# Optimization experiments

Measured on AMD Instinct MI355X. Metric: run time of the kernel, lower is better.

The kernel has to match this reference:

```python
import jax, jax.numpy as jnp
import numpy as np

NEG_SLOPE = 0.2  # PyG GATConv default LeakyReLU slope
EPS = 1e-16


def gat_layer(x, W, a_src, a_dst, bias, src, dst, heads, out_dim, concat):
    N = x.shape[0]
    h = (x @ W).reshape(N, heads, out_dim)          # [N,H,C]
    alpha_src = (h * a_src).sum(-1)                  # [N,H]
    alpha_dst = (h * a_dst).sum(-1)                  # [N,H]
    e = jax.nn.leaky_relu(alpha_src[src] + alpha_dst[dst], NEG_SLOPE)  # [E,H]
    # segment softmax over incoming edges of each destination node
    m = jax.ops.segment_max(e, dst, num_segments=N)  # [N,H]
    p = jnp.exp(e - m[dst])
    denom = jax.ops.segment_sum(p, dst, num_segments=N)
    alpha = p / (denom[dst] + EPS)                   # [E,H]
    # scatter-aggregate messages to destinations
    out = jax.ops.segment_sum(alpha[:, :, None] * h[src], dst, num_segments=N)  # [N,H,C]
    out = out.reshape(N, heads * out_dim) if concat else out.mean(axis=1)
    return out + bias


def setup_inputs() -> dict:
    N, E, F_IN, NC = 100000, 1600000, 512, 10
    key = jax.random.key(0)
    ks = jax.random.split(key, 9)
    return {
        "x": jax.random.normal(ks[0], (N, F_IN), jnp.float32),
        "W1": jax.random.normal(ks[1], (F_IN, 64), jnp.float32) * (1.0 / np.sqrt(F_IN)),
        "att_src1": jax.random.normal(ks[2], (1, 8, 8), jnp.float32) * 0.1,
        "att_dst1": jax.random.normal(ks[3], (1, 8, 8), jnp.float32) * 0.1,
        "b1": jnp.zeros((64,), jnp.float32),
        "W2": jax.random.normal(ks[4], (64, NC), jnp.float32) * (1.0 / 8.0),
        "att_src2": jax.random.normal(ks[5], (1, 1, NC), jnp.float32) * 0.1,
        "att_dst2": jax.random.normal(ks[6], (1, 1, NC), jnp.float32) * 0.1,
        "b2": jnp.zeros((NC,), jnp.float32),
        "edge_index": jax.random.randint(ks[7], (2, E), 0, N, jnp.int64),
    }


def reference(x, W1, att_src1, att_dst1, b1, W2, att_src2, att_dst2, b2, edge_index):
    N = x.shape[0]
    # add self-loops (PyG GATConv add_self_loops=True default)
    loop = jnp.arange(N, dtype=edge_index.dtype)
    src = jnp.concatenate([edge_index[0], loop])
    dst = jnp.concatenate([edge_index[1], loop])
    h = gat_layer(x, W1, att_src1, att_dst1, b1, src, dst, heads=8, out_dim=8, concat=True)
    h = jax.nn.elu(h)
    nc = W2.shape[1]
    out = gat_layer(h, W2, att_src2, att_dst2, b2, src, dst, heads=1, out_dim=nc, concat=False)
    return jax.nn.log_softmax(out, axis=1)
```

## Files before the change

### kernel.cpp

```cpp
#include <hip/hip_runtime.h>
#include <math.h>

#define NEG 0.2f

typedef __bf16 bf16x8 __attribute__((ext_vector_type(8)));
typedef __bf16 bf16x4 __attribute__((ext_vector_type(4)));
typedef float  f32x4  __attribute__((ext_vector_type(4)));

__global__ void histw1_k(const int* __restrict__ ei, int E, int Nn,
                         int* __restrict__ deg, int* __restrict__ rank,
                         const float* __restrict__ W1, __bf16* __restrict__ W1b)
{
    if (blockIdx.x < 16) {
        int i = blockIdx.x * 256 + threadIdx.x;
        int n = i & 63;
        int k0 = (i >> 6) * 8;
#pragma unroll
        for (int j = 0; j < 8; ++j)
            W1b[(size_t)i * 8 + j] = (__bf16)W1[(size_t)(k0 + j) * 64 + n];
        return;
    }
    int e = (blockIdx.x - 16) * 256 + threadIdx.x;
    int Ep = E + Nn;
    if (e >= Ep) return;
    int d = (e < E) ? ei[E + e] : e - E;
    rank[e] = atomicAdd(&deg[d], 1);
}

__global__ void scan_a_k(const int* __restrict__ deg, int Nn, int* __restrict__ bsum)
{
    __shared__ int tmp[256];
    int t = threadIdx.x;
    int base = blockIdx.x * 1024 + t * 4;
    int s = 0;
#pragma unroll
    for (int j = 0; j < 4; ++j) { int i = base + j; if (i < Nn) s += deg[i]; }
    tmp[t] = s;
    __syncthreads();
    for (int off = 1; off < 256; off <<= 1) {
        int a = (t >= off) ? tmp[t - off] : 0;
        __syncthreads();
        tmp[t] += a;
        __syncthreads();
    }
    if (t == 255) bsum[blockIdx.x] = tmp[255];
}

__global__ void scan_b_k(int* __restrict__ bsum, int nb)
{
    __shared__ int tmp[256];
    int t = threadIdx.x;
    int v = (t < nb) ? bsum[t] : 0;
    tmp[t] = v;
    __syncthreads();
    for (int off = 1; off < 256; off <<= 1) {
        int a = (t >= off) ? tmp[t - off] : 0;
        __syncthreads();
        tmp[t] += a;
        __syncthreads();
    }
    if (t < nb) bsum[t] = tmp[t] - v;
}

__global__ void scan_c_k(const int* __restrict__ deg, int Nn, const int* __restrict__ boff,
                         int* __restrict__ rowptr)
{
    __shared__ int tmp[256];
    int t = threadIdx.x;
    int base = blockIdx.x * 1024 + t * 4;
    int v[4];
    int s = 0;
#pragma unroll
    for (int j = 0; j < 4; ++j) {
        int i = base + j;
        v[j] = (i < Nn) ? deg[i] : 0;
        s += v[j];
    }
    tmp[t] = s;
    __syncthreads();
    for (int off = 1; off < 256; off <<= 1) {
        int a = (t >= off) ? tmp[t - off] : 0;
        __syncthreads();
        tmp[t] += a;
        __syncthreads();
    }
    int excl = boff[blockIdx.x] + tmp[t] - s;
#pragma unroll
    for (int j = 0; j < 4; ++j) {
        int i = base + j;
        if (i < Nn) {
            rowptr[i] = excl;
            excl += v[j];
            if (i == Nn - 1) rowptr[Nn] = excl;
        }
    }
}

__global__ __launch_bounds__(256, 4) void scatgemm_k(
    const float* __restrict__ x, const __bf16* __restrict__ W1b,
    const float* __restrict__ asrc, const float* __restrict__ adst,
    __bf16* __restrict__ h1b, float* __restrict__ as1, float* __restrict__ ad1,
    const int* __restrict__ ei, int E,
    const int* __restrict__ rowptr, const int* __restrict__ rank,
    int* __restrict__ csr, int Nn, int nbG)
{
    if ((int)blockIdx.x >= nbG) {
        int e = ((int)blockIdx.x - nbG) * 256 + threadIdx.x;
        int Ep = E + Nn;
        if (e >= Ep) return;
        int s, d;
        if (e < E) { s = ei[e]; d = ei[E + e]; } else { s = d = e - E; }
        csr[rowptr[d] + rank[e]] = s;
        return;
    }
    int t = threadIdx.x;
    int wave = t >> 6, lane = t & 63;
    int lm = lane & 15, lk = lane >> 4;
    int rowa = blockIdx.x * 64 + wave * 16 + lm;
    const float* xrow = x + (size_t)(rowa < Nn ? rowa : 0) * 512;
    f32x4 acc[4] = {};
#pragma unroll
    for (int ch = 0; ch < 16; ++ch) {
        float4 a0 = *(const float4*)(xrow + ch * 32 + lk * 8);
        float4 a1 = *(const float4*)(xrow + ch * 32 + lk * 8 + 4);
        bf16x8 af;
        af[0] = (__bf16)a0.x; af[1] = (__bf16)a0.y;
        af[2] = (__bf16)a0.z; af[3] = (__bf16)a0.w;
        af[4] = (__bf16)a1.x; af[5] = (__bf16)a1.y;
        af[6] = (__bf16)a1.z; af[7] = (__bf16)a1.w;
#pragma unroll
        for (int nt = 0; nt < 4; ++nt) {
            bf16x8 bf = *(const bf16x8*)(W1b + ((size_t)((ch * 4 + lk) * 64) + nt * 16 + lm) * 8);
            acc[nt] = __builtin_amdgcn_mfma_f32_16x16x32_bf16(af, bf, acc[nt], 0, 0, 0);
        }
    }
    int rowbase = blockIdx.x * 64 + wave * 16 + lk * 4;
#pragma unroll
    for (int nt = 0; nt < 4; ++nt) {
#pragma unroll
        for (int j = 0; j < 4; ++j) {
            int gr = rowbase + j;
            if (gr < Nn) h1b[(size_t)gr * 64 + nt * 16 + lm] = (__bf16)acc[nt][j];
        }
    }
#pragma unroll
    for (int nt = 0; nt < 4; ++nt) {
        float ws = asrc[nt * 16 + lm];
        float wd = adst[nt * 16 + lm];
#pragma unroll
        for (int j = 0; j < 4; ++j) {
            float sv = acc[nt][j] * ws;
            float dv = acc[nt][j] * wd;
            sv += __shfl_xor(sv, 1); dv += __shfl_xor(dv, 1);
            sv += __shfl_xor(sv, 2); dv += __shfl_xor(dv, 2);
            sv += __shfl_xor(sv, 4); dv += __shfl_xor(dv, 4);
            int gr = rowbase + j;
            if ((lm & 7) == 0 && gr < Nn) {
                int hh = nt * 2 + (lm >> 3);
                as1[(size_t)gr * 8 + hh] = sv;
                ad1[(size_t)gr * 8 + hh] = dv;
            }
        }
    }
}

__global__ __launch_bounds__(256, 4) void agg1n_k(const int* __restrict__ csr,
                                                  const int* __restrict__ rowptr,
                                                  const float* __restrict__ as1,
                                                  const float* __restrict__ ad1,
                                                  const __bf16* __restrict__ h1b,
                                                  const float* __restrict__ b1,
                                                  const float* __restrict__ W2,
                                                  const float* __restrict__ as2w,
                                                  const float* __restrict__ ad2w,
                                                  float* __restrict__ h2,
                                                  float* __restrict__ as2,
                                                  float* __restrict__ ad2, int Nn)
{
    __shared__ float W2s[640];
    for (int i = threadIdx.x; i < 640; i += 256) W2s[i] = W2[i];
    __syncthreads();

    int wid = (blockIdx.x * 256 + threadIdx.x) >> 6;
    if (wid >= Nn) return;
    int lane = threadIdx.x & 63;
    int sub = lane >> 4;
    int c4 = lane & 15;
    int h = c4 >> 1;
    float adv = ad1[wid * 8 + h];
    int start = rowptr[wid];
    int len = rowptr[wid + 1] - start;
    float accp = 0.f;
    float4 accv = make_float4(0.f, 0.f, 0.f, 0.f);
    int i = sub;
    for (; i + 12 < len; i += 16) {
        int s0 = csr[start + i];
        int s1 = csr[start + i + 4];
        int s2 = csr[start + i + 8];
        int s3 = csr[start + i + 12];
        float e0 = as1[s0 * 8 + h] + adv;
        float e1 = as1[s1 * 8 + h] + adv;
        float e2 = as1[s2 * 8 + h] + adv;
        float e3 = as1[s3 * 8 + h] + adv;
        bf16x4 hv0 = *(const bf16x4*)(h1b + (size_t)s0 * 64 + c4 * 4);
        bf16x4 hv1 = *(const bf16x4*)(h1b + (size_t)s1 * 64 + c4 * 4);
        bf16x4 hv2 = *(const bf16x4*)(h1b + (size_t)s2 * 64 + c4 * 4);
        bf16x4 hv3 = *(const bf16x4*)(h1b + (size_t)s3 * 64 + c4 * 4);
        e0 = e0 > 0.f ? e0 : NEG * e0;
        e1 = e1 > 0.f ? e1 : NEG * e1;
        e2 = e2 > 0.f ? e2 : NEG * e2;
        e3 = e3 > 0.f ? e3 : NEG * e3;
        float p0 = __expf(e0), p1 = __expf(e1), p2 = __expf(e2), p3 = __expf(e3);
        accp += (p0 + p1) + (p2 + p3);
        accv.x += p0 * (float)hv0[0] + p1 * (float)hv1[0] + p2 * (float)hv2[0] + p3 * (float)hv3[0];
        accv.y += p0 * (float)hv0[1] + p1 * (float)hv1[1] + p2 * (float)hv2[1] + p3 * (float)hv3[1];
        accv.z += p0 * (float)hv0[2] + p1 * (float)hv1[2] + p2 * (float)hv2[2] + p3 * (float)hv3[2];
        accv.w += p0 * (float)hv0[3] + p1 * (float)hv1[3] + p2 * (float)hv2[3] + p3 * (float)hv3[3];
    }
    for (; i < len; i += 4) {
        int s0 = csr[start + i];
        float e0 = as1[s0 * 8 + h] + adv;
        bf16x4 hv0 = *(const bf16x4*)(h1b + (size_t)s0 * 64 + c4 * 4);
        e0 = e0 > 0.f ? e0 : NEG * e0;
        float p0 = __expf(e0);
        accp += p0;
        accv.x += p0 * (float)hv0[0];
        accv.y += p0 * (float)hv0[1];
        accv.z += p0 * (float)hv0[2];
        accv.w += p0 * (float)hv0[3];
    }
    accp   += __shfl_xor(accp, 16);
    accv.x += __shfl_xor(accv.x, 16);
    accv.y += __shfl_xor(accv.y, 16);
    accv.z += __shfl_xor(accv.z, 16);
    accv.w += __shfl_xor(accv.w, 16);
    accp   += __shfl_xor(accp, 32);
    accv.x += __shfl_xor(accv.x, 32);
    accv.y += __shfl_xor(accv.y, 32);
    accv.z += __shfl_xor(accv.z, 32);
    accv.w += __shfl_xor(accv.w, 32);

    float inv = 1.f / (accp + 1e-16f);
    float4 b = *(const float4*)(b1 + c4 * 4);
    float g0 = accv.x * inv + b.x; g0 = g0 > 0.f ? g0 : expm1f(g0);
    float g1 = accv.y * inv + b.y; g1 = g1 > 0.f ? g1 : expm1f(g1);
    float g2 = accv.z * inv + b.z; g2 = g2 > 0.f ? g2 : expm1f(g2);
    float g3 = accv.w * inv + b.w; g3 = g3 > 0.f ? g3 : expm1f(g3);
    int k0 = c4 * 4;
    float aj[10];
#pragma unroll
    for (int j = 0; j < 10; ++j)
        aj[j] = g0 * W2s[(k0 + 0) * 10 + j] + g1 * W2s[(k0 + 1) * 10 + j]
              + g2 * W2s[(k0 + 2) * 10 + j] + g3 * W2s[(k0 + 3) * 10 + j];
#pragma unroll
    for (int m = 1; m <= 8; m <<= 1) {
#pragma unroll
        for (int j = 0; j < 10; ++j) aj[j] += __shfl_xor(aj[j], m);
    }
    if (lane == 0) {
        float s2 = 0.f, d2 = 0.f;
#pragma unroll
        for (int j = 0; j < 10; ++j) { s2 += aj[j] * as2w[j]; d2 += aj[j] * ad2w[j]; }
        *(float4*)(h2 + (size_t)wid * 16 + 0) = make_float4(aj[0], aj[1], aj[2], aj[3]);
        *(float4*)(h2 + (size_t)wid * 16 + 4) = make_float4(aj[4], aj[5], aj[6], aj[7]);
        h2[(size_t)wid * 16 + 8] = aj[8];
        h2[(size_t)wid * 16 + 9] = aj[9];
        as2[wid] = s2;
        ad2[wid] = d2;
    }
}

__global__ __launch_bounds__(256) void agg2l_k(const int* __restrict__ csr,
                                               const int* __restrict__ rowptr,
                                               const float* __restrict__ as2,
                                               const float* __restrict__ ad2,
                                               const float* __restrict__ h2,
                                               const float* __restrict__ b2,
                                               float* __restrict__ out, int Nn)
{
    int wid = (blockIdx.x * 256 + threadIdx.x) >> 6;
    if (wid >= Nn) return;
    int lane = threadIdx.x & 63;
    int sub = lane >> 4;
    int c = lane & 15;
    float adv = ad2[wid];
    int start = rowptr[wid];
    int len = rowptr[wid + 1] - start;
    float accp = 0.f, accv = 0.f;
    int i = sub;
    for (; i + 12 < len; i += 16) {
        int s0 = csr[start + i];
        int s1 = csr[start + i + 4];
        int s2 = csr[start + i + 8];
        int s3 = csr[start + i + 12];
        float e0 = as2[s0] + adv;
        float e1 = as2[s1] + adv;
        float e2 = as2[s2] + adv;
        float e3 = as2[s3] + adv;
        float v0 = (c < 10) ? h2[(size_t)s0 * 16 + c] : 0.f;
        float v1 = (c < 10) ? h2[(size_t)s1 * 16 + c] : 0.f;
        float v2 = (c < 10) ? h2[(size_t)s2 * 16 + c] : 0.f;
        float v3 = (c < 10) ? h2[(size_t)s3 * 16 + c] : 0.f;
        e0 = e0 > 0.f ? e0 : NEG * e0;
        e1 = e1 > 0.f ? e1 : NEG * e1;
        e2 = e2 > 0.f ? e2 : NEG * e2;
        e3 = e3 > 0.f ? e3 : NEG * e3;
        float p0 = __expf(e0), p1 = __expf(e1), p2 = __expf(e2), p3 = __expf(e3);
        accp += (p0 + p1) + (p2 + p3);
        accv += p0 * v0 + p1 * v1 + p2 * v2 + p3 * v3;
    }
    for (; i < len; i += 4) {
        int s0 = csr[start + i];
        float e0 = as2[s0] + adv;
        float v0 = (c < 10) ? h2[(size_t)s0 * 16 + c] : 0.f;
        e0 = e0 > 0.f ? e0 : NEG * e0;
        float p0 = __expf(e0);
        accp += p0;
        accv += p0 * v0;
    }
    accp += __shfl_xor(accp, 16);
    accv += __shfl_xor(accv, 16);
    accp += __shfl_xor(accp, 32);
    accv += __shfl_xor(accv, 32);

    float z = (c < 10) ? accv / (accp + 1e-16f) + b2[c] : -1e30f;
    float m = z;
    m = fmaxf(m, __shfl_xor(m, 1));
    m = fmaxf(m, __shfl_xor(m, 2));
    m = fmaxf(m, __shfl_xor(m, 4));
    m = fmaxf(m, __shfl_xor(m, 8));
    float p = (c < 10) ? expf(z - m) : 0.f;
    p += __shfl_xor(p, 1);
    p += __shfl_xor(p, 2);
    p += __shfl_xor(p, 4);
    p += __shfl_xor(p, 8);
    float lse = m + logf(p);
    if (sub == 0 && c < 10)
        out[(size_t)wid * 10 + c] = z - lse;
}

extern "C" void kernel_launch(void* const* d_in, const int* in_sizes, int n_in,
                              void* d_out, int out_size, void* d_ws, size_t ws_size,
                              hipStream_t stream)
{
    const float* x     = (const float*)d_in[0];
    const float* W1    = (const float*)d_in[1];
    const float* asrc1 = (const float*)d_in[2];
    const float* adst1 = (const float*)d_in[3];
    const float* b1    = (const float*)d_in[4];
    const float* W2    = (const float*)d_in[5];
    const float* asrc2 = (const float*)d_in[6];
    const float* adst2 = (const float*)d_in[7];
    const float* b2    = (const float*)d_in[8];
    const int*   ei    = (const int*)d_in[9];
    float* out = (float*)d_out;

    int F  = in_sizes[1] / 64;
    int Nn = in_sizes[0] / F;
    int E  = in_sizes[9] / 2;
    int Ep = E + Nn;
    int nb = (Nn + 1023) / 1024;

    float* f = (float*)d_ws;
    __bf16* w1b = (__bf16*)f;  f += 512 * 64 / 2;
    __bf16* h1b = (__bf16*)f;  f += (size_t)Nn * 32;
    float* as1  = f;  f += (size_t)Nn * 8;
    float* ad1  = f;  f += (size_t)Nn * 8;
    float* h2   = f;  f += (size_t)Nn * 16;
    float* as2  = f;  f += Nn;
    float* ad2  = f;  f += Nn;
    int* ip = (int*)f;
    int* deg    = ip;  ip += Nn;
    int* rowptr = ip;  ip += Nn + 1;
    int* bsum   = ip;  ip += 256;
    int* rank   = ip;  ip += Ep;
    int* csr    = ip;  ip += Ep;

    int nbG = (Nn + 63) / 64;
    int nbS = (Ep + 255) / 256;

    hipMemsetAsync(deg, 0, (size_t)Nn * sizeof(int), stream);
    histw1_k<<<16 + nbS, 256, 0, stream>>>(ei, E, Nn, deg, rank, W1, w1b);

    scan_a_k<<<nb, 256, 0, stream>>>(deg, Nn, bsum);
    scan_b_k<<<1, 256, 0, stream>>>(bsum, nb);
    scan_c_k<<<nb, 256, 0, stream>>>(deg, Nn, bsum, rowptr);

    scatgemm_k<<<nbG + nbS, 256, 0, stream>>>(x, w1b, asrc1, adst1, h1b, as1, ad1,
                                              ei, E, rowptr, rank, csr, Nn, nbG);

    agg1n_k<<<(Nn + 3) / 4, 256, 0, stream>>>(csr, rowptr, as1, ad1, h1b,
                                              b1, W2, asrc2, adst2, h2, as2, ad2, Nn);

    agg2l_k<<<(Nn + 3) / 4, 256, 0, stream>>>(csr, rowptr, as2, ad2, h2, b2, out, Nn);
}
```

Baseline: 570.4 us.

## Widen per-lane gather vectors in aggregation kernels and split fused scatter/GEMM launch

Both aggregation kernels now give each lane a wider slice of the feature row, 8 bf16 values in layer 1 and 2 floats in layer 2. Eight edges are processed in parallel per wave, with a single masked 4-way unrolled loop replacing the unrolled loop plus tail loop. This is meant to cut the number of gather instructions and improve memory-level parallelism on the random neighbor reads, at the cost of more registers and wasted work on masked tail edges. The previously fused CSR-scatter/GEMM launch is split into two separate kernels, which removes the branch divergence between block types but adds a launch and loses the overlap between them.

```diff
diff --git a/kernel.cpp b/kernel.cpp
--- a/kernel.cpp
+++ b/kernel.cpp
@@ -4,7 +4,6 @@
 #define NEG 0.2f
 
 typedef __bf16 bf16x8 __attribute__((ext_vector_type(8)));
-typedef __bf16 bf16x4 __attribute__((ext_vector_type(4)));
 typedef float  f32x4  __attribute__((ext_vector_type(4)));
 
 __global__ void histw1_k(const int* __restrict__ ei, int E, int Nn,
@@ -96,23 +95,26 @@
     }
 }
 
-__global__ __launch_bounds__(256, 4) void scatgemm_k(
-    const float* __restrict__ x, const __bf16* __restrict__ W1b,
-    const float* __restrict__ asrc, const float* __restrict__ adst,
-    __bf16* __restrict__ h1b, float* __restrict__ as1, float* __restrict__ ad1,
-    const int* __restrict__ ei, int E,
-    const int* __restrict__ rowptr, const int* __restrict__ rank,
-    int* __restrict__ csr, int Nn, int nbG)
-{
-    if ((int)blockIdx.x >= nbG) {
-        int e = ((int)blockIdx.x - nbG) * 256 + threadIdx.x;
-        int Ep = E + Nn;
-        if (e >= Ep) return;
-        int s, d;
-        if (e < E) { s = ei[e]; d = ei[E + e]; } else { s = d = e - E; }
-        csr[rowptr[d] + rank[e]] = s;
-        return;
-    }
+__global__ void scat2_k(const int* __restrict__ ei, int E, int Nn,
+                        const int* __restrict__ rowptr, const int* __restrict__ rank,
+                        int* __restrict__ csr)
+{
+    int e = blockIdx.x * 256 + threadIdx.x;
+    int Ep = E + Nn;
+    if (e >= Ep) return;
+    int s, d;
+    if (e < E) { s = ei[e]; d = ei[E + e]; } else { s = d = e - E; }
+    csr[rowptr[d] + rank[e]] = s;
+}
+
+__global__ __launch_bounds__(256, 4) void gemm1a_k(const float* __restrict__ x,
+                                                   const __bf16* __restrict__ W1b,
+                                                   const float* __restrict__ asrc,
+                                                   const float* __restrict__ adst,
+                                                   __bf16* __restrict__ h1b,
+                                                   float* __restrict__ as1,
+                                                   float* __restrict__ ad1, int Nn)
+{
     int t = threadIdx.x;
     int wave = t >> 6, lane = t & 63;
     int lm = lane & 15, lk = lane >> 4;
@@ -184,76 +186,74 @@
     int wid = (blockIdx.x * 256 + threadIdx.x) >> 6;
     if (wid >= Nn) return;
     int lane = threadIdx.x & 63;
-    int sub = lane >> 4;
-    int c4 = lane & 15;
-    int h = c4 >> 1;
-    float adv = ad1[wid * 8 + h];
+    int sub = lane >> 3;
+    int c8  = lane & 7;
+    float advh = ad1[(size_t)wid * 8 + c8];
     int start = rowptr[wid];
     int len = rowptr[wid + 1] - start;
     float accp = 0.f;
-    float4 accv = make_float4(0.f, 0.f, 0.f, 0.f);
-    int i = sub;
-    for (; i + 12 < len; i += 16) {
-        int s0 = csr[start + i];
-        int s1 = csr[start + i + 4];
-        int s2 = csr[start + i + 8];
-        int s3 = csr[start + i + 12];
-        float e0 = as1[s0 * 8 + h] + adv;
-        float e1 = as1[s1 * 8 + h] + adv;
-        float e2 = as1[s2 * 8 + h] + adv;
-        float e3 = as1[s3 * 8 + h] + adv;
-        bf16x4 hv0 = *(const bf16x4*)(h1b + (size_t)s0 * 64 + c4 * 4);
-        bf16x4 hv1 = *(const bf16x4*)(h1b + (size_t)s1 * 64 + c4 * 4);
-        bf16x4 hv2 = *(const bf16x4*)(h1b + (size_t)s2 * 64 + c4 * 4);
-        bf16x4 hv3 = *(const bf16x4*)(h1b + (size_t)s3 * 64 + c4 * 4);
+    float accv[8] = {};
+    for (int i = sub; i < len; i += 32) {
+        int idx = start + i;
+        bool k1 = i + 8 < len, k2 = i + 16 < len, k3 = i + 24 < len;
+        int s0 = csr[idx];
+        int s1 = csr[idx + (k1 ? 8 : 0)];
+        int s2 = csr[idx + (k2 ? 16 : 0)];
+        int s3 = csr[idx + (k3 ? 24 : 0)];
+        float e0 = as1[(size_t)s0 * 8 + c8] + advh;
+        float e1 = as1[(size_t)s1 * 8 + c8] + advh;
+        float e2 = as1[(size_t)s2 * 8 + c8] + advh;
+        float e3 = as1[(size_t)s3 * 8 + c8] + advh;
+        bf16x8 hv0 = *(const bf16x8*)(h1b + (size_t)s0 * 64 + c8 * 8);
+        bf16x8 hv1 = *(const bf16x8*)(h1b + (size_t)s1 * 64 + c8 * 8);
+        bf16x8 hv2 = *(const bf16x8*)(h1b + (size_t)s2 * 64 + c8 * 8);
+        bf16x8 hv3 = *(const bf16x8*)(h1b + (size_t)s3 * 64 + c8 * 8);
         e0 = e0 > 0.f ? e0 : NEG * e0;
         e1 = e1 > 0.f ? e1 : NEG * e1;
         e2 = e2 > 0.f ? e2 : NEG * e2;
         e3 = e3 > 0.f ? e3 : NEG * e3;
+        if (!k1) e1 = -1e30f;
+        if (!k2) e2 = -1e30f;
+        if (!k3) e3 = -1e30f;
         float p0 = __expf(e0), p1 = __expf(e1), p2 = __expf(e2), p3 = __expf(e3);
         accp += (p0 + p1) + (p2 + p3);
-        accv.x += p0 * (float)hv0[0] + p1 * (float)hv1[0] + p2 * (float)hv2[0] + p3 * (float)hv3[0];
-        accv.y += p0 * (float)hv0[1] + p1 * (float)hv1[1] + p2 * (float)hv2[1] + p3 * (float)hv3[1];
-        accv.z += p0 * (float)hv0[2] + p1 * (float)hv1[2] + p2 * (float)hv2[2] + p3 * (float)hv3[2];
-        accv.w += p0 * (float)hv0[3] + p1 * (float)hv1[3] + p2 * (float)hv2[3] + p3 * (float)hv3[3];
-    }
-    for (; i < len; i += 4) {
-        int s0 = csr[start + i];
-        float e0 = as1[s0 * 8 + h] + adv;
-        bf16x4 hv0 = *(const bf16x4*)(h1b + (size_t)s0 * 64 + c4 * 4);
-        e0 = e0 > 0.f ? e0 : NEG * e0;
-        float p0 = __expf(e0);
-        accp += p0;
-        accv.x += p0 * (float)hv0[0];
-        accv.y += p0 * (float)hv0[1];
-        accv.z += p0 * (float)hv0[2];
-        accv.w += p0 * (float)hv0[3];
-    }
-    accp   += __shfl_xor(accp, 16);
-    accv.x += __shfl_xor(accv.x, 16);
-    accv.y += __shfl_xor(accv.y, 16);
-    accv.z += __shfl_xor(accv.z, 16);
-    accv.w += __shfl_xor(accv.w, 16);
-    accp   += __shfl_xor(accp, 32);
-    accv.x += __shfl_xor(accv.x, 32);
-    accv.y += __shfl_xor(accv.y, 32);
-    accv.z += __shfl_xor(accv.z, 32);
-    accv.w += __shfl_xor(accv.w, 32);
+#pragma unroll
+        for (int c = 0; c < 8; ++c)
+            accv[c] += p0 * (float)hv0[c] + p1 * (float)hv1[c]
+                     + p2 * (float)hv2[c] + p3 * (float)hv3[c];
+    }
+#pragma unroll
+    for (int m = 8; m <= 32; m <<= 1) {
+        accp += __shfl_xor(accp, m);
+#pragma unroll
+        for (int c = 0; c < 8; ++c) accv[c] += __shfl_xor(accv[c], m);
+    }
 
     float inv = 1.f / (accp + 1e-16f);
-    float4 b = *(const float4*)(b1 + c4 * 4);
-    float g0 = accv.x * inv + b.x; g0 = g0 > 0.f ? g0 : expm1f(g0);
-    float g1 = accv.y * inv + b.y; g1 = g1 > 0.f ? g1 : expm1f(g1);
-    float g2 = accv.z * inv + b.z; g2 = g2 > 0.f ? g2 : expm1f(g2);
-    float g3 = accv.w * inv + b.w; g3 = g3 > 0.f ? g3 : expm1f(g3);
-    int k0 = c4 * 4;
+    float4 ba = *(const float4*)(b1 + c8 * 8);
+    float4 bb = *(const float4*)(b1 + c8 * 8 + 4);
+    float g[8];
+    g[0] = accv[0] * inv + ba.x;
+    g[1] = accv[1] * inv + ba.y;
+    g[2] = accv[2] * inv + ba.z;
+    g[3] = accv[3] * inv + ba.w;
+    g[4] = accv[4] * inv + bb.x;
+    g[5] = accv[5] * inv + bb.y;
+    g[6] = accv[6] * inv + bb.z;
+    g[7] = accv[7] * inv + bb.w;
+#pragma unroll
+    for (int c = 0; c < 8; ++c) g[c] = g[c] > 0.f ? g[c] : expm1f(g[c]);
+    int k0 = c8 * 8;
     float aj[10];
 #pragma unroll
-    for (int j = 0; j < 10; ++j)
-        aj[j] = g0 * W2s[(k0 + 0) * 10 + j] + g1 * W2s[(k0 + 1) * 10 + j]
-              + g2 * W2s[(k0 + 2) * 10 + j] + g3 * W2s[(k0 + 3) * 10 + j];
-#pragma unroll
-    for (int m = 1; m <= 8; m <<= 1) {
+    for (int j = 0; j < 10; ++j) {
+        float a = 0.f;
+#pragma unroll
+        for (int c = 0; c < 8; ++c) a += g[c] * W2s[(k0 + c) * 10 + j];
+        aj[j] = a;
+    }
+#pragma unroll
+    for (int m = 1; m <= 4; m <<= 1) {
 #pragma unroll
         for (int j = 0; j < 10; ++j) aj[j] += __shfl_xor(aj[j], m);
     }
@@ -270,73 +270,73 @@
     }
 }
 
-__global__ __launch_bounds__(256) void agg2l_k(const int* __restrict__ csr,
-                                               const int* __restrict__ rowptr,
-                                               const float* __restrict__ as2,
-                                               const float* __restrict__ ad2,
-                                               const float* __restrict__ h2,
-                                               const float* __restrict__ b2,
-                                               float* __restrict__ out, int Nn)
+__global__ __launch_bounds__(256, 4) void agg2l_k(const int* __restrict__ csr,
+                                                  const int* __restrict__ rowptr,
+                                                  const float* __restrict__ as2,
+                                                  const float* __restrict__ ad2,
+                                                  const float* __restrict__ h2,
+                                                  const float* __restrict__ b2,
+                                                  float* __restrict__ out, int Nn)
 {
     int wid = (blockIdx.x * 256 + threadIdx.x) >> 6;
     if (wid >= Nn) return;
     int lane = threadIdx.x & 63;
-    int sub = lane >> 4;
-    int c = lane & 15;
+    int sub = lane >> 3;
+    int c2 = lane & 7;
+    bool act = (c2 < 5);
     float adv = ad2[wid];
     int start = rowptr[wid];
     int len = rowptr[wid + 1] - start;
-    float accp = 0.f, accv = 0.f;
-    int i = sub;
-    for (; i + 12 < len; i += 16) {
-        int s0 = csr[start + i];
-        int s1 = csr[start + i + 4];
-        int s2 = csr[start + i + 8];
-        int s3 = csr[start + i + 12];
+    float accp = 0.f, av0 = 0.f, av1 = 0.f;
+    const float2 z2 = make_float2(0.f, 0.f);
+    for (int i = sub; i < len; i += 32) {
+        int idx = start + i;
+        bool k1 = i + 8 < len, k2 = i + 16 < len, k3 = i + 24 < len;
+        int s0 = csr[idx];
+        int s1 = csr[idx + (k1 ? 8 : 0)];
+        int s2 = csr[idx + (k2 ? 16 : 0)];
+        int s3 = csr[idx + (k3 ? 24 : 0)];
         float e0 = as2[s0] + adv;
         float e1 = as2[s1] + adv;
         float e2 = as2[s2] + adv;
         float e3 = as2[s3] + adv;
-        float v0 = (c < 10) ? h2[(size_t)s0 * 16 + c] : 0.f;
-        float v1 = (c < 10) ? h2[(size_t)s1 * 16 + c] : 0.f;
-        float v2 = (c < 10) ? h2[(size_t)s2 * 16 + c] : 0.f;
-        float v3 = (c < 10) ? h2[(size_t)s3 * 16 + c] : 0.f;
+        float2 v0 = act ? *(const float2*)(h2 + (size_t)s0 * 16 + c2 * 2) : z2;
+        float2 v1 = act ? *(const float2*)(h2 + (size_t)s1 * 16 + c2 * 2) : z2;
+        float2 v2 = act ? *(const float2*)(h2 + (size_t)s2 * 16 + c2 * 2) : z2;
+        float2 v3 = act ? *(const float2*)(h2 + (size_t)s3 * 16 + c2 * 2) : z2;
         e0 = e0 > 0.f ? e0 : NEG * e0;
         e1 = e1 > 0.f ? e1 : NEG * e1;
         e2 = e2 > 0.f ? e2 : NEG * e2;
         e3 = e3 > 0.f ? e3 : NEG * e3;
+        if (!k1) e1 = -1e30f;
+        if (!k2) e2 = -1e30f;
+        if (!k3) e3 = -1e30f;
         float p0 = __expf(e0), p1 = __expf(e1), p2 = __expf(e2), p3 = __expf(e3);
         accp += (p0 + p1) + (p2 + p3);
-        accv += p0 * v0 + p1 * v1 + p2 * v2 + p3 * v3;
-    }
-    for (; i < len; i += 4) {
-        int s0 = csr[start + i];
-        float e0 = as2[s0] + adv;
-        float v0 = (c < 10) ? h2[(size_t)s0 * 16 + c] : 0.f;
-        e0 = e0 > 0.f ? e0 : NEG * e0;
-        float p0 = __expf(e0);
-        accp += p0;
-        accv += p0 * v0;
-    }
-    accp += __shfl_xor(accp, 16);
-    accv += __shfl_xor(accv, 16);
-    accp += __shfl_xor(accp, 32);
-    accv += __shfl_xor(accv, 32);
-
-    float z = (c < 10) ? accv / (accp + 1e-16f) + b2[c] : -1e30f;
-    float m = z;
+        av0 += p0 * v0.x + p1 * v1.x + p2 * v2.x + p3 * v3.x;
+        av1 += p0 * v0.y + p1 * v1.y + p2 * v2.y + p3 * v3.y;
+    }
+#pragma unroll
+    for (int m = 8; m <= 32; m <<= 1) {
+        accp += __shfl_xor(accp, m);
+        av0  += __shfl_xor(av0, m);
+        av1  += __shfl_xor(av1, m);
+    }
+
+    float inv = 1.f / (accp + 1e-16f);
+    float z0 = act ? av0 * inv + b2[c2 * 2]     : -1e30f;
+    float z1 = act ? av1 * inv + b2[c2 * 2 + 1] : -1e30f;
+    float m = fmaxf(z0, z1);
     m = fmaxf(m, __shfl_xor(m, 1));
     m = fmaxf(m, __shfl_xor(m, 2));
     m = fmaxf(m, __shfl_xor(m, 4));
-    m = fmaxf(m, __shfl_xor(m, 8));
-    float p = (c < 10) ? expf(z - m) : 0.f;
-    p += __shfl_xor(p, 1);
-    p += __shfl_xor(p, 2);
-    p += __shfl_xor(p, 4);
-    p += __shfl_xor(p, 8);
-    float lse = m + logf(p);
-    if (sub == 0 && c < 10)
-        out[(size_t)wid * 10 + c] = z - lse;
+    float ps = act ? expf(z0 - m) + expf(z1 - m) : 0.f;
+    ps += __shfl_xor(ps, 1);
+    ps += __shfl_xor(ps, 2);
+    ps += __shfl_xor(ps, 4);
+    float lse = m + logf(ps);
+    if (sub == 0 && act)
+        *(float2*)(out + (size_t)wid * 10 + c2 * 2) = make_float2(z0 - lse, z1 - lse);
 }
 
 extern "C" void kernel_launch(void* const* d_in, const int* in_sizes, int n_in,
@@ -376,7 +376,6 @@
     int* rank   = ip;  ip += Ep;
     int* csr    = ip;  ip += Ep;
 
-    int nbG = (Nn + 63) / 64;
     int nbS = (Ep + 255) / 256;
 
     hipMemsetAsync(deg, 0, (size_t)Nn * sizeof(int), stream);
@@ -386,8 +385,9 @@
     scan_b_k<<<1, 256, 0, stream>>>(bsum, nb);
     scan_c_k<<<nb, 256, 0, stream>>>(deg, Nn, bsum, rowptr);
 
-    scatgemm_k<<<nbG + nbS, 256, 0, stream>>>(x, w1b, asrc1, adst1, h1b, as1, ad1,
-                                              ei, E, rowptr, rank, csr, Nn, nbG);
+    scat2_k<<<nbS, 256, 0, stream>>>(ei, E, Nn, rowptr, rank, csr);
+
+    gemm1a_k<<<(Nn + 63) / 64, 256, 0, stream>>>(x, w1b, asrc1, adst1, h1b, as1, ad1, Nn);
 
     agg1n_k<<<(Nn + 3) / 4, 256, 0, stream>>>(csr, rowptr, as1, ad1, h1b,
                                               b1, W2, asrc2, adst2, h2, as2, ad2, Nn);
```

Result: slower. 587.0 us (+2.9%).
